# Performance work log

Hardware: AMD Instinct MI355X
Metric: run time of the kernel (lower is better)

## Reference

```python
import jax, jax.numpy as jnp
import numpy as np

HIDDEN = 512
ATT = 512
B, S = 32, 2048


def setup_inputs() -> dict:
    key = jax.random.key(0)
    ks = jax.random.split(key, 9)
    enc_output = jax.random.normal(ks[0], (B, S, 2 * HIDDEN), dtype=jnp.float32)
    decoder_hidden = jax.random.normal(ks[1], (B, HIDDEN), dtype=jnp.float32)
    masks = jax.random.randint(ks[2], (B, S, 1), 0, 2).astype(jnp.bool_)
    # Learned params (init_weights style: uniform(-0.1, 0.1), zero bias)
    W_enc = jax.random.uniform(ks[3], (2 * HIDDEN, ATT), minval=-0.1, maxval=0.1, dtype=jnp.float32)
    b_enc = jnp.zeros((ATT,), dtype=jnp.float32)
    W_dec = jax.random.uniform(ks[4], (HIDDEN, ATT), minval=-0.1, maxval=0.1, dtype=jnp.float32)
    b_dec = jnp.zeros((ATT,), dtype=jnp.float32)
    W_att = jax.random.uniform(ks[5], (ATT, 1), minval=-0.1, maxval=0.1, dtype=jnp.float32)
    b_att = jnp.zeros((1,), dtype=jnp.float32)
    return {
        "enc_output": enc_output,
        "decoder_hidden": decoder_hidden,
        "masks": masks,
        "W_enc": W_enc,
        "b_enc": b_enc,
        "W_dec": W_dec,
        "b_dec": b_dec,
        "W_att": W_att,
        "b_att": b_att,
    }


def reference(enc_output, decoder_hidden, masks, W_enc, b_enc, W_dec, b_dec, W_att, b_att):
    # encoder_att: [B, S, A]
    encoder_att = jnp.einsum("bse,ea->bsa", enc_output, W_enc) + b_enc
    # decoder_att: [B, A]
    decoder_att = decoder_hidden @ W_dec + b_dec
    # scores: [B, S, 1]
    scores = jnp.tanh(encoder_att + decoder_att[:, None, :]) @ W_att + b_att
    scores = jnp.where(masks, -jnp.inf, scores)
    att_weights = jax.nn.softmax(scores, axis=1)  # softmax over seq dim
    # context over encoder_att (note: original weights encoder_att, not enc_output)
    att_context_vector = jnp.sum(encoder_att * att_weights, axis=1)  # [B, A]
    return att_context_vector
```

## Files before the change

kernel.cpp:

```cpp
#include <hip/hip_runtime.h>
#include <math.h>

#define B_  32
#define S_  2048
#define E_  1024
#define A_  512
#define H_  512

#define MB   128
#define NCH  (S_ / MB)
#define KT   32
#define NK   (E_ / KT)

typedef __bf16 bf16;
typedef __attribute__((ext_vector_type(8))) __bf16 bf16x8;
typedef __attribute__((ext_vector_type(4))) float  f32x4;

typedef const __attribute__((address_space(1))) unsigned int g_u32;
typedef __attribute__((address_space(3))) unsigned int lds_u32;

__device__ __forceinline__ void glds16(const void* g, void* l) {
    __builtin_amdgcn_global_load_lds((g_u32*)g, (lds_u32*)l, 16, 0, 0);
}

__device__ __forceinline__ float fast_tanh(float x) {
    x = fminf(fmaxf(x, -15.f), 15.f);
    const float e = __expf(2.f * x);
    return (e - 1.f) / (e + 1.f);
}

__global__ __launch_bounds__(256)
void prep_kernel(const float* __restrict__ Wenc,
                 const float* __restrict__ dh,
                 const float* __restrict__ Wdec,
                 const float* __restrict__ bdec,
                 bf16* __restrict__ Whi, bf16* __restrict__ Wlo,
                 float* __restrict__ dp) {
    const int t = threadIdx.x;
    if (blockIdx.x < 128) {
        __shared__ float tile[64][65];
        const int kb = blockIdx.x >> 3;
        const int ab = blockIdx.x & 7;
        const int k0 = kb * 64, a0 = ab * 64;
#pragma unroll
        for (int p = 0; p < 8; ++p) {
            const int kk = p * 8 + (t >> 5);
            const int aa = (t & 31) * 2;
            const float2 v = *(const float2*)&Wenc[(size_t)(k0 + kk) * A_ + a0 + aa];
            tile[kk][aa]     = v.x;
            tile[kk][aa + 1] = v.y;
        }
        __syncthreads();
        const int aa  = t >> 2;
        const int kk0 = (t & 3) * 16;
        bf16x8 hv0, hv1, lv0, lv1;
#pragma unroll
        for (int j = 0; j < 16; ++j) {
            const float x = tile[kk0 + j][aa];
            const bf16 h = (bf16)x;
            const bf16 l = (bf16)(x - (float)h);
            if (j < 8) { hv0[j] = h; lv0[j] = l; }
            else       { hv1[j - 8] = h; lv1[j - 8] = l; }
        }
        bf16* dh_ = Whi + (size_t)(a0 + aa) * E_ + k0 + kk0;
        bf16* dl_ = Wlo + (size_t)(a0 + aa) * E_ + k0 + kk0;
        *(bf16x8*)dh_ = hv0; *((bf16x8*)dh_ + 1) = hv1;
        *(bf16x8*)dl_ = lv0; *((bf16x8*)dl_ + 1) = lv1;
    } else {
        __shared__ float dhl[64];
        const int idx = blockIdx.x - 128;
        const int b   = idx >> 3;
        const int seg = idx & 7;
        if (t < 64) dhl[t] = dh[b * H_ + seg * 64 + t];
        __syncthreads();
        const int a0 = t, a1 = t + 256;
        float acc0 = 0.f, acc1 = 0.f;
        const float* Wrow = Wdec + (size_t)(seg * 64) * A_;
#pragma unroll 8
        for (int h = 0; h < 64; ++h) {
            const float s = dhl[h];
            acc0 += s * Wrow[h * A_ + a0];
            acc1 += s * Wrow[h * A_ + a1];
        }
        if (seg == 0) { acc0 += bdec[a0]; acc1 += bdec[a1]; }
        dp[(size_t)(seg * B_ + b) * A_ + a0] = acc0;
        dp[(size_t)(seg * B_ + b) * A_ + a1] = acc1;
    }
}

__global__ __launch_bounds__(512, 2)
void fused_kernel(const float* __restrict__ enc,
                  const int*   __restrict__ masks,
                  const bf16*  __restrict__ Whi_g,
                  const bf16*  __restrict__ Wlo_g,
                  const float* __restrict__ benc,
                  const float* __restrict__ Watt,
                  const float* __restrict__ batt,
                  const float* __restrict__ dp,
                  float* __restrict__ pm,
                  float* __restrict__ pl,
                  float* __restrict__ pctx) {
    __shared__ union {
        struct {
            __align__(16) bf16 Whi[A_ * KT];
            __align__(16) bf16 Wlo[A_ * KT];
            __align__(16) bf16 Ab[2][2][MB * KT];
        } k;
        struct {
            float decl[A_], wattl[A_], bencl[A_];
            float red[MB * 8];
            float score[MB], p[MB];
            int   mask[MB];
        } e;
    } sm;

    const int t    = threadIdx.x;
    const int wv   = t >> 6;
    const int L    = t & 63;
    const int quad = L >> 4;
    const int colL = L & 15;
    const int b    = blockIdx.x >> 4;
    const int ch   = blockIdx.x & 15;
    const int s0   = ch * MB;

    const float* encB = enc + ((size_t)(b * S_ + s0)) * E_;

    f32x4 acc[8][4];
#pragma unroll
    for (int mt = 0; mt < 8; ++mt)
#pragma unroll
        for (int nt = 0; nt < 4; ++nt) acc[mt][nt] = (f32x4){0.f, 0.f, 0.f, 0.f};

    const int arow = t >> 2;
    const int akq  = t & 3;
    const int a_wr = ((arow >> 4) * 512) + akq * 128 +
                     (((arow & 15) ^ (akq << 2)) * 8);
    const float* aptr = encB + (size_t)arow * E_ + akq * 8;
    const int a_rd = quad * 128 + (((L & 15) ^ (quad << 2)) * 8);

    const size_t wg0 = (size_t)((wv * 4) * 16 + colL) * E_ + quad * 8;

    float4 cA = *(const float4*)(aptr);
    float4 cB = *(const float4*)(aptr + 4);
#pragma unroll
    for (int i = 0; i < 4; ++i) {
        const int I = wv * 4 + i;
        const size_t goff = wg0 + (size_t)(i * 16) * E_;
        glds16(Whi_g + goff, &sm.k.Whi[I * 512]);
        glds16(Wlo_g + goff, &sm.k.Wlo[I * 512]);
    }
    {
        const float xs[8] = {cA.x, cA.y, cA.z, cA.w, cB.x, cB.y, cB.z, cB.w};
        bf16x8 hv, lv;
#pragma unroll
        for (int j = 0; j < 8; ++j) {
            const bf16 h = (bf16)xs[j];
            hv[j] = h; lv[j] = (bf16)(xs[j] - (float)h);
        }
        *(bf16x8*)&sm.k.Ab[0][0][a_wr] = hv;
        *(bf16x8*)&sm.k.Ab[0][1][a_wr] = lv;
    }
    __syncthreads();

    bf16x8 bh[4], bl[4];
#pragma unroll
    for (int nt = 0; nt < 4; ++nt) {
        bh[nt] = *(const bf16x8*)&sm.k.Whi[(wv * 4 + nt) * 512 + L * 8];
        bl[nt] = *(const bf16x8*)&sm.k.Wlo[(wv * 4 + nt) * 512 + L * 8];
    }

    for (int kt = 0; kt < NK; ++kt) {
        __syncthreads();
        const bool more = (kt + 1 < NK);
        if (more) {
            const size_t kadd = (size_t)(kt + 1) * KT;
#pragma unroll
            for (int i = 0; i < 4; ++i) {
                const int I = wv * 4 + i;
                const size_t goff = wg0 + (size_t)(i * 16) * E_ + kadd;
                glds16(Whi_g + goff, &sm.k.Whi[I * 512]);
                glds16(Wlo_g + goff, &sm.k.Wlo[I * 512]);
            }
            const float* np = aptr + (size_t)(kt + 1) * KT;
            cA = *(const float4*)(np);
            cB = *(const float4*)(np + 4);
        }

        const bf16* Ahi = sm.k.Ab[kt & 1][0];
        const bf16* Alo = sm.k.Ab[kt & 1][1];
#pragma unroll
        for (int mt = 0; mt < 8; ++mt) {
            const bf16x8 ah = *(const bf16x8*)&Ahi[mt * 512 + a_rd];
            const bf16x8 al = *(const bf16x8*)&Alo[mt * 512 + a_rd];
#pragma unroll
            for (int nt = 0; nt < 4; ++nt) {
                acc[mt][nt] = __builtin_amdgcn_mfma_f32_16x16x32_bf16(ah, bh[nt], acc[mt][nt], 0, 0, 0);
                acc[mt][nt] = __builtin_amdgcn_mfma_f32_16x16x32_bf16(al, bh[nt], acc[mt][nt], 0, 0, 0);
                acc[mt][nt] = __builtin_amdgcn_mfma_f32_16x16x32_bf16(ah, bl[nt], acc[mt][nt], 0, 0, 0);
            }
        }

        if (more) {
            const float xs[8] = {cA.x, cA.y, cA.z, cA.w, cB.x, cB.y, cB.z, cB.w};
            bf16x8 hv, lv;
#pragma unroll
            for (int j = 0; j < 8; ++j) {
                const bf16 h = (bf16)xs[j];
                hv[j] = h; lv[j] = (bf16)(xs[j] - (float)h);
            }
            *(bf16x8*)&sm.k.Ab[(kt + 1) & 1][0][a_wr] = hv;
            *(bf16x8*)&sm.k.Ab[(kt + 1) & 1][1][a_wr] = lv;
        }

        __syncthreads();
        if (more) {
#pragma unroll
            for (int nt = 0; nt < 4; ++nt) {
                bh[nt] = *(const bf16x8*)&sm.k.Whi[(wv * 4 + nt) * 512 + L * 8];
                bl[nt] = *(const bf16x8*)&sm.k.Wlo[(wv * 4 + nt) * 512 + L * 8];
            }
        }
    }

    {
        float d = 0.f;
#pragma unroll
        for (int g = 0; g < 8; ++g) d += dp[(size_t)(g * B_ + b) * A_ + t];
        sm.e.decl[t]  = d;
        sm.e.wattl[t] = Watt[t];
        sm.e.bencl[t] = benc[t];
        if (t < MB) sm.e.mask[t] = masks[(size_t)b * S_ + s0 + t];
    }
    __syncthreads();

    float sp[8][4];
#pragma unroll
    for (int mt = 0; mt < 8; ++mt)
#pragma unroll
        for (int r = 0; r < 4; ++r) sp[mt][r] = 0.f;

#pragma unroll
    for (int nt = 0; nt < 4; ++nt) {
        const int cg = wv * 64 + nt * 16 + colL;
        const float bv  = sm.e.bencl[cg];
        const float dv  = sm.e.decl[cg];
        const float wav = sm.e.wattl[cg];
#pragma unroll
        for (int mt = 0; mt < 8; ++mt)
#pragma unroll
            for (int r = 0; r < 4; ++r) {
                const float ea = acc[mt][nt][r] + bv;
                acc[mt][nt][r] = ea;
                sp[mt][r] += fast_tanh(ea + dv) * wav;
            }
    }
#pragma unroll
    for (int d = 1; d < 16; d <<= 1)
#pragma unroll
        for (int mt = 0; mt < 8; ++mt)
#pragma unroll
            for (int r = 0; r < 4; ++r)
                sp[mt][r] += __shfl_xor(sp[mt][r], d);
    if (colL == 0) {
#pragma unroll
        for (int mt = 0; mt < 8; ++mt)
#pragma unroll
            for (int r = 0; r < 4; ++r)
                sm.e.red[(mt * 16 + quad * 4 + r) * 8 + wv] = sp[mt][r];
    }
    __syncthreads();

    if (t < MB) {
        float s = 0.f;
#pragma unroll
        for (int j = 0; j < 8; ++j) s += sm.e.red[t * 8 + j];
        sm.e.score[t] = s + batt[0];
    }
    __syncthreads();

    float m_loc = -1e30f;
    for (int r = 0; r < MB; ++r)
        if (!sm.e.mask[r]) m_loc = fmaxf(m_loc, sm.e.score[r]);
    if (t < MB) sm.e.p[t] = sm.e.mask[t] ? 0.f : __expf(sm.e.score[t] - m_loc);
    __syncthreads();

    float ctxl[4] = {0.f, 0.f, 0.f, 0.f};
#pragma unroll
    for (int mt = 0; mt < 8; ++mt)
#pragma unroll
        for (int r = 0; r < 4; ++r) {
            const float p = sm.e.p[mt * 16 + quad * 4 + r];
#pragma unroll
            for (int nt = 0; nt < 4; ++nt) ctxl[nt] += p * acc[mt][nt][r];
        }
#pragma unroll
    for (int nt = 0; nt < 4; ++nt) {
        ctxl[nt] += __shfl_xor(ctxl[nt], 16);
        ctxl[nt] += __shfl_xor(ctxl[nt], 32);
    }
    if (quad == 0) {
#pragma unroll
        for (int nt = 0; nt < 4; ++nt)
            pctx[(size_t)blockIdx.x * A_ + wv * 64 + nt * 16 + colL] = ctxl[nt];
    }
    if (t == 0) {
        float l = 0.f;
        for (int r = 0; r < MB; ++r) l += sm.e.p[r];
        pm[blockIdx.x] = m_loc;
        pl[blockIdx.x] = l;
    }
}

__global__ __launch_bounds__(512)
void combine_kernel(const float* __restrict__ pm,
                    const float* __restrict__ pl,
                    const float* __restrict__ pctx,
                    float* __restrict__ out) {
    const int b = blockIdx.x;
    const int t = threadIdx.x;
    float m_g = -1e30f;
    for (int c = 0; c < NCH; ++c) m_g = fmaxf(m_g, pm[b * NCH + c]);
    float L = 0.f;
    for (int c = 0; c < NCH; ++c)
        L += pl[b * NCH + c] * __expf(pm[b * NCH + c] - m_g);
    const float inv = 1.f / L;
    float s = 0.f;
    for (int c = 0; c < NCH; ++c)
        s += pctx[((size_t)b * NCH + c) * A_ + t] * __expf(pm[b * NCH + c] - m_g);
    out[b * A_ + t] = s * inv;
}

extern "C" void kernel_launch(void* const* d_in, const int* in_sizes, int n_in,
                              void* d_out, int out_size, void* d_ws, size_t ws_size,
                              hipStream_t stream) {
    const float* enc  = (const float*)d_in[0];
    const float* dh   = (const float*)d_in[1];
    const int*   mks  = (const int*)  d_in[2];
    const float* Wenc = (const float*)d_in[3];
    const float* benc = (const float*)d_in[4];
    const float* Wdec = (const float*)d_in[5];
    const float* bdec = (const float*)d_in[6];
    const float* Watt = (const float*)d_in[7];
    const float* batt = (const float*)d_in[8];
    float* out = (float*)d_out;

    float* ws   = (float*)d_ws;
    float* pm   = ws;
    float* pl   = pm + B_ * NCH;
    float* pctx = pl + B_ * NCH;
    float* dp   = pctx + (size_t)B_ * NCH * A_;
    bf16*  Whi  = (bf16*)(dp + 8 * B_ * A_);
    bf16*  Wlo  = Whi + (size_t)A_ * E_;
    (void)in_sizes; (void)n_in; (void)out_size; (void)ws_size;

    prep_kernel<<<384, 256, 0, stream>>>(Wenc, dh, Wdec, bdec, Whi, Wlo, dp);
    fused_kernel<<<B_ * NCH, 512, 0, stream>>>(
        enc, mks, Whi, Wlo, benc, Watt, batt, dp, pm, pl, pctx);
    combine_kernel<<<B_, 512, 0, stream>>>(pm, pl, pctx, out);
}
```

Measured before the change: 522.8 us.

## Load weight fragments directly into registers and deepen enc prefetch pipeline

Replaces the LDS staging of the hi/lo bf16 weight tiles (global_load_lds plus LDS reads) with direct per-wave global loads into double-buffered registers. The K loop is manually unrolled by two with ping-pong register sets, enc rows are prefetched two steps ahead, and only one barrier per step remains, using a raw s_barrier after an lgkmcnt wait. This frees LDS and removes one sync per iteration. In exchange it raises register pressure at 2 waves/EU occupancy and relies on the L2/cache to serve repeated weight reads.

```diff
diff --git a/kernel.cpp b/kernel.cpp
--- a/kernel.cpp
+++ b/kernel.cpp
@@ -15,13 +15,6 @@
 typedef __bf16 bf16;
 typedef __attribute__((ext_vector_type(8))) __bf16 bf16x8;
 typedef __attribute__((ext_vector_type(4))) float  f32x4;
-
-typedef const __attribute__((address_space(1))) unsigned int g_u32;
-typedef __attribute__((address_space(3))) unsigned int lds_u32;
-
-__device__ __forceinline__ void glds16(const void* g, void* l) {
-    __builtin_amdgcn_global_load_lds((g_u32*)g, (lds_u32*)l, 16, 0, 0);
-}
 
 __device__ __forceinline__ float fast_tanh(float x) {
     x = fminf(fmaxf(x, -15.f), 15.f);
@@ -102,8 +95,6 @@
                   float* __restrict__ pctx) {
     __shared__ union {
         struct {
-            __align__(16) bf16 Whi[A_ * KT];
-            __align__(16) bf16 Wlo[A_ * KT];
             __align__(16) bf16 Ab[2][2][MB * KT];
         } k;
         struct {
@@ -138,19 +129,23 @@
     const float* aptr = encB + (size_t)arow * E_ + akq * 8;
     const int a_rd = quad * 128 + (((L & 15) ^ (quad << 2)) * 8);
 
-    const size_t wg0 = (size_t)((wv * 4) * 16 + colL) * E_ + quad * 8;
-
-    float4 cA = *(const float4*)(aptr);
-    float4 cB = *(const float4*)(aptr + 4);
-#pragma unroll
-    for (int i = 0; i < 4; ++i) {
-        const int I = wv * 4 + i;
-        const size_t goff = wg0 + (size_t)(i * 16) * E_;
-        glds16(Whi_g + goff, &sm.k.Whi[I * 512]);
-        glds16(Wlo_g + goff, &sm.k.Wlo[I * 512]);
-    }
+    const bf16* wHi = Whi_g + (size_t)(wv * 64 + colL) * E_ + quad * 8;
+    const bf16* wLo = Wlo_g + (size_t)(wv * 64 + colL) * E_ + quad * 8;
+
+    bf16x8 bh0[4], bl0[4], bh1[4], bl1[4];
+    float4 cA0, cB0, cA1, cB1;
+
+    cA0 = *(const float4*)(aptr);
+    cB0 = *(const float4*)(aptr + 4);
+#pragma unroll
+    for (int nt = 0; nt < 4; ++nt) {
+        bh0[nt] = *(const bf16x8*)(wHi + (size_t)nt * (16 * E_));
+        bl0[nt] = *(const bf16x8*)(wLo + (size_t)nt * (16 * E_));
+    }
+    cA1 = *(const float4*)(aptr + KT);
+    cB1 = *(const float4*)(aptr + KT + 4);
     {
-        const float xs[8] = {cA.x, cA.y, cA.z, cA.w, cB.x, cB.y, cB.z, cB.w};
+        const float xs[8] = {cA0.x, cA0.y, cA0.z, cA0.w, cB0.x, cB0.y, cB0.z, cB0.w};
         bf16x8 hv, lv;
 #pragma unroll
         for (int j = 0; j < 8; ++j) {
@@ -160,68 +155,67 @@
         *(bf16x8*)&sm.k.Ab[0][0][a_wr] = hv;
         *(bf16x8*)&sm.k.Ab[0][1][a_wr] = lv;
     }
-    __syncthreads();
-
-    bf16x8 bh[4], bl[4];
-#pragma unroll
-    for (int nt = 0; nt < 4; ++nt) {
-        bh[nt] = *(const bf16x8*)&sm.k.Whi[(wv * 4 + nt) * 512 + L * 8];
-        bl[nt] = *(const bf16x8*)&sm.k.Wlo[(wv * 4 + nt) * 512 + L * 8];
-    }
-
-    for (int kt = 0; kt < NK; ++kt) {
-        __syncthreads();
-        const bool more = (kt + 1 < NK);
-        if (more) {
-            const size_t kadd = (size_t)(kt + 1) * KT;
-#pragma unroll
-            for (int i = 0; i < 4; ++i) {
-                const int I = wv * 4 + i;
-                const size_t goff = wg0 + (size_t)(i * 16) * E_ + kadd;
-                glds16(Whi_g + goff, &sm.k.Whi[I * 512]);
-                glds16(Wlo_g + goff, &sm.k.Wlo[I * 512]);
-            }
-            const float* np = aptr + (size_t)(kt + 1) * KT;
-            cA = *(const float4*)(np);
-            cB = *(const float4*)(np + 4);
-        }
-
-        const bf16* Ahi = sm.k.Ab[kt & 1][0];
-        const bf16* Alo = sm.k.Ab[kt & 1][1];
-#pragma unroll
-        for (int mt = 0; mt < 8; ++mt) {
-            const bf16x8 ah = *(const bf16x8*)&Ahi[mt * 512 + a_rd];
-            const bf16x8 al = *(const bf16x8*)&Alo[mt * 512 + a_rd];
-#pragma unroll
-            for (int nt = 0; nt < 4; ++nt) {
-                acc[mt][nt] = __builtin_amdgcn_mfma_f32_16x16x32_bf16(ah, bh[nt], acc[mt][nt], 0, 0, 0);
-                acc[mt][nt] = __builtin_amdgcn_mfma_f32_16x16x32_bf16(al, bh[nt], acc[mt][nt], 0, 0, 0);
-                acc[mt][nt] = __builtin_amdgcn_mfma_f32_16x16x32_bf16(ah, bl[nt], acc[mt][nt], 0, 0, 0);
-            }
-        }
-
-        if (more) {
-            const float xs[8] = {cA.x, cA.y, cA.z, cA.w, cB.x, cB.y, cB.z, cB.w};
-            bf16x8 hv, lv;
-#pragma unroll
-            for (int j = 0; j < 8; ++j) {
-                const bf16 h = (bf16)xs[j];
-                hv[j] = h; lv[j] = (bf16)(xs[j] - (float)h);
-            }
-            *(bf16x8*)&sm.k.Ab[(kt + 1) & 1][0][a_wr] = hv;
-            *(bf16x8*)&sm.k.Ab[(kt + 1) & 1][1][a_wr] = lv;
-        }
-
-        __syncthreads();
-        if (more) {
-#pragma unroll
-            for (int nt = 0; nt < 4; ++nt) {
-                bh[nt] = *(const bf16x8*)&sm.k.Whi[(wv * 4 + nt) * 512 + L * 8];
-                bl[nt] = *(const bf16x8*)&sm.k.Wlo[(wv * 4 + nt) * 512 + L * 8];
-            }
-        }
-    }
-
+    asm volatile("s_waitcnt lgkmcnt(0)" ::: "memory");
+    __builtin_amdgcn_s_barrier();
+    asm volatile("" ::: "memory");
+
+#define STEP(KT_, BH, BL, BHN, BLN, PA, PB, QA, QB)                            \
+    {                                                                          \
+        const int ktn_ = (KT_) + 1;                                            \
+        if (ktn_ < NK) {                                                       \
+            _Pragma("unroll")                                                  \
+            for (int nt = 0; nt < 4; ++nt) {                                   \
+                BHN[nt] = *(const bf16x8*)(wHi + (size_t)nt * (16 * E_) +      \
+                                           (size_t)ktn_ * KT);                 \
+                BLN[nt] = *(const bf16x8*)(wLo + (size_t)nt * (16 * E_) +      \
+                                           (size_t)ktn_ * KT);                 \
+            }                                                                  \
+        }                                                                      \
+        if ((KT_) + 2 < NK) {                                                  \
+            const float* np_ = aptr + (size_t)((KT_) + 2) * KT;                \
+            QA = *(const float4*)(np_);                                        \
+            QB = *(const float4*)(np_ + 4);                                    \
+        }                                                                      \
+        const bf16* Ahi_ = sm.k.Ab[(KT_) & 1][0];                              \
+        const bf16* Alo_ = sm.k.Ab[(KT_) & 1][1];                              \
+        _Pragma("unroll")                                                      \
+        for (int mt = 0; mt < 8; ++mt) {                                       \
+            const bf16x8 ah = *(const bf16x8*)&Ahi_[mt * 512 + a_rd];          \
+            const bf16x8 al = *(const bf16x8*)&Alo_[mt * 512 + a_rd];          \
+            _Pragma("unroll")                                                  \
+            for (int nt = 0; nt < 4; ++nt) {                                   \
+                acc[mt][nt] = __builtin_amdgcn_mfma_f32_16x16x32_bf16(         \
+                    ah, BH[nt], acc[mt][nt], 0, 0, 0);                         \
+                acc[mt][nt] = __builtin_amdgcn_mfma_f32_16x16x32_bf16(         \
+                    al, BH[nt], acc[mt][nt], 0, 0, 0);                         \
+                acc[mt][nt] = __builtin_amdgcn_mfma_f32_16x16x32_bf16(         \
+                    ah, BL[nt], acc[mt][nt], 0, 0, 0);                         \
+            }                                                                  \
+        }                                                                      \
+        if (ktn_ < NK) {                                                       \
+            const float xs_[8] = {PA.x, PA.y, PA.z, PA.w,                      \
+                                  PB.x, PB.y, PB.z, PB.w};                     \
+            bf16x8 hv_, lv_;                                                   \
+            _Pragma("unroll")                                                  \
+            for (int j = 0; j < 8; ++j) {                                      \
+                const bf16 h_ = (bf16)xs_[j];                                  \
+                hv_[j] = h_; lv_[j] = (bf16)(xs_[j] - (float)h_);              \
+            }                                                                  \
+            *(bf16x8*)&sm.k.Ab[ktn_ & 1][0][a_wr] = hv_;                       \
+            *(bf16x8*)&sm.k.Ab[ktn_ & 1][1][a_wr] = lv_;                       \
+            asm volatile("s_waitcnt lgkmcnt(0)" ::: "memory");                 \
+            __builtin_amdgcn_s_barrier();                                      \
+            asm volatile("" ::: "memory");                                     \
+        }                                                                      \
+    }
+
+    for (int kt = 0; kt < NK; kt += 2) {
+        STEP(kt,     bh0, bl0, bh1, bl1, cA1, cB1, cA0, cB0);
+        STEP(kt + 1, bh1, bl1, bh0, bl0, cA0, cB0, cA1, cB1);
+    }
+#undef STEP
+
+    __syncthreads();
     {
         float d = 0.f;
 #pragma unroll
```

Measured after the change: 534.1 us. +2.2%, slower.
